# Kernel optimization log

Measured on AMD Instinct MI355X. Metric: run time of the kernel, lower is better.

The kernel has to match this reference:

```python
import jax, jax.numpy as jnp
import numpy as np

N_NODES = 50000
N_EDGES = 800000
D_IN = 64
D_OUT = 64


def setup_inputs() -> dict:
    key = jax.random.key(0)
    k1, k2, k3, k4, k5, k6 = jax.random.split(key, 6)
    feat = jax.random.normal(k1, (N_NODES, D_IN), dtype=jnp.float32)
    edge_weight = jax.random.uniform(k2, (N_EDGES, 1), dtype=jnp.float32)
    # xavier_uniform bound for [D_IN, D_OUT]
    bound = float(np.sqrt(6.0 / (D_IN + D_OUT)))
    W1 = jax.random.uniform(k3, (D_IN, D_OUT), minval=-bound, maxval=bound, dtype=jnp.float32)
    W2 = jax.random.uniform(k4, (D_IN, D_OUT), minval=-bound, maxval=bound, dtype=jnp.float32)
    src = jax.random.randint(k5, (N_EDGES,), 0, N_NODES, dtype=jnp.int64)
    dst = jax.random.randint(k6, (N_EDGES,), 0, N_NODES, dtype=jnp.int64)
    return {"feat": feat, "edge_weight": edge_weight, "W1": W1, "W2": W2, "src": src, "dst": dst}


def reference(feat, edge_weight, W1, W2, src, dst):
    # message: u_sub_e -> src feature minus (broadcast) edge weight  [E, D_IN]
    msgs = feat[src] - edge_weight
    # sum aggregation over destination nodes  [N, D_IN]
    agg = jax.ops.segment_sum(msgs, dst, num_segments=feat.shape[0])
    # dual dense projections; no activation (activation=None)
    rst = jnp.matmul(feat, W1) + jnp.matmul(agg, W2)
    return rst
```

## Files before the change

### kernel.cpp

```cpp
#include <hip/hip_runtime.h>

#define NN 50000
#define NE 800000
#define D  64
#define NB 782
#define EBLK 2048
#define NEB 391
#define CAPB 1280

typedef unsigned int u32;
typedef unsigned short u16;
typedef unsigned long long u64;
typedef __attribute__((ext_vector_type(8))) short bf16x8;
typedef __attribute__((ext_vector_type(4))) float f32x4;
typedef __attribute__((ext_vector_type(2))) float f32x2;

__device__ __forceinline__ int wave_incl_scan(int v, int lane) {
    #pragma unroll
    for (int off = 1; off < 64; off <<= 1) {
        int t = __shfl_up(v, off);
        if (lane >= off) v += t;
    }
    return v;
}

__device__ __forceinline__ u32 f2bf(float x) {
    u32 u = __float_as_uint(x);
    return (u + 0x7fffu + ((u >> 16) & 1u)) >> 16;
}

__device__ __forceinline__ bf16x8 as_bf8(uint4 u) {
    union { uint4 a; bf16x8 b; } x; x.a = u; return x.b;
}

__device__ __forceinline__ u32 pk_fp8x4(float a, float b, float c, float d) {
    int w = __builtin_amdgcn_cvt_pk_fp8_f32(a, b, 0, false);
    w = __builtin_amdgcn_cvt_pk_fp8_f32(c, d, w, true);
    return (u32)w;
}

__device__ __forceinline__ uint2 fp8x4_to_bf16x4(u32 uu) {
    f32x2 lo = __builtin_amdgcn_cvt_pk_f32_fp8((int)uu, false);
    f32x2 hi = __builtin_amdgcn_cvt_pk_f32_fp8((int)uu, true);
    uint2 r;
    r.x = f2bf(lo.x) | (f2bf(lo.y) << 16);
    r.y = f2bf(hi.x) | (f2bf(hi.y) << 16);
    return r;
}

__global__ __launch_bounds__(256) void kb_scatter(const int* __restrict__ src,
                                                  const int* __restrict__ dst,
                                                  const float* __restrict__ ew,
                                                  const float* __restrict__ feat,
                                                  u32* __restrict__ cursor,
                                                  u64* __restrict__ sorted,
                                                  uint2* __restrict__ featb8)
{
    __shared__ u32 h[NB], eb[NB], ctr[NB], gb[NB];
    __shared__ u64 buf[EBLK];
    int tid = threadIdx.x;
    for (int i = tid; i < NB; i += 256) h[i] = 0;
    __syncthreads();
    int base = blockIdx.x * EBLK;
    int n = min(EBLK, NE - base);

    u32 rd[8], rs[8], rw[8];
    #pragma unroll
    for (int j = 0; j < 8; ++j) {
        int k = tid + j * 256;
        if (k < n) {
            int e = base + k;
            rd[j] = (u32)dst[e];
            rs[j] = (u32)src[e];
            rw[j] = __float_as_uint(ew[e]);
            atomicAdd(&h[rd[j] >> 6], 1u);
        }
    }
    __syncthreads();
    if (tid < 64) {
        u32 carry = 0;
        for (int c = 0; c < 13; ++c) {
            int idx = c * 64 + tid;
            u32 v = (idx < NB) ? h[idx] : 0;
            int incl = wave_incl_scan((int)v, tid);
            if (idx < NB) { u32 e = (u32)incl - v + carry; eb[idx] = e; ctr[idx] = e; }
            carry += (u32)__shfl(incl, 63);
        }
    }
    __syncthreads();
    for (int i = tid; i < NB; i += 256) gb[i] = atomicAdd(&cursor[i], h[i]);
    __syncthreads();
    #pragma unroll
    for (int j = 0; j < 8; ++j) {
        int k = tid + j * 256;
        if (k < n) {
            u64 rec = ((u64)((rd[j] << 16) | rs[j]) << 32) | (u64)rw[j];
            u32 p = atomicAdd(&ctr[rd[j] >> 6], 1u);
            buf[p] = rec;
        }
    }
    __syncthreads();
    for (int k = tid; k < n; k += 256) {
        u64 rec = buf[k];
        u32 bin = (u32)(rec >> 54);
        u32 idx = gb[bin] + (u32)k - eb[bin];
        if (idx < CAPB) sorted[(size_t)bin * CAPB + idx] = rec;
    }

    int cbase = blockIdx.x * 1024;
    const float4* f4 = (const float4*)feat;
    #pragma unroll
    for (int j = 0; j < 4; ++j) {
        int i = cbase + j * 256 + tid;
        if (i < NN * D / 8) {
            float4 a = f4[2 * i], b = f4[2 * i + 1];
            uint2 p8;
            p8.x = pk_fp8x4(a.x, a.y, a.z, a.w);
            p8.y = pk_fp8x4(b.x, b.y, b.z, b.w);
            featb8[i] = p8;
        }
    }
}

__global__ __launch_bounds__(1024) void kcgg(
    const u64* __restrict__ sorted,
    const u32* __restrict__ cursor,
    const u32* __restrict__ fb8,
    const float* __restrict__ W1,
    const float* __restrict__ W2,
    float* __restrict__ out)
{
    __shared__ u32 hcnt[64], hbase[65], ctr[64];
    __shared__ u16 bufS[CAPB];
    __shared__ u32 bufWf[CAPB];
    __shared__ u16 aggT[64][72];
    __shared__ u16 wT[64][136];
    __shared__ float csp[4][64];
    __shared__ float csum[64];
    __shared__ float sWs[64];

    const int tid = threadIdx.x;
    const int bin = blockIdx.x;
    const int n = min((int)cursor[bin], CAPB);
    const size_t rbase = (size_t)bin * CAPB;

    for (int i = tid; i < 8192; i += 1024) {
        int k = i >> 6, c = i & 63;
        float v = (k < 64) ? W1[i] : W2[i - 4096];
        wT[c][k] = (u16)f2bf(v);
    }
    if (tid < 256) {
        int c = tid & 63, kq = tid >> 6;
        float s = 0.f;
        for (int k = kq * 16; k < kq * 16 + 16; ++k) s += W2[k * 64 + c];
        csp[kq][c] = s;
    }
    if (tid < 64) hcnt[tid] = 0;
    __syncthreads();
    if (tid < 64) csum[tid] = csp[0][tid] + csp[1][tid] + csp[2][tid] + csp[3][tid];
    for (int k = tid; k < n; k += 1024)
        atomicAdd(&hcnt[(int)(sorted[rbase + k] >> 48) & 63], 1u);
    __syncthreads();
    if (tid < 64) {
        u32 v = hcnt[tid];
        int incl = wave_incl_scan((int)v, tid);
        u32 ex = (u32)incl - v;
        hbase[tid] = ex; ctr[tid] = ex;
        if (tid == 63) hbase[64] = (u32)incl;
    }
    __syncthreads();
    for (int k = tid; k < n; k += 1024) {
        u64 rec = sorted[rbase + k];
        u32 p = atomicAdd(&ctr[(int)(rec >> 48) & 63], 1u);
        bufS[p]  = (u16)(rec >> 32);
        bufWf[p] = (u32)rec;
    }
    __syncthreads();

    const int w    = tid >> 6;
    const int lane = tid & 63;
    const int g    = lane >> 4;
    const int li   = lane & 15;
    const int ln   = w * 4 + g;

    int e   = (int)hbase[ln];
    int end = (int)hbase[ln + 1];

    if (li == 0) {
        float s = 0.f;
        for (int j = e; j < end; ++j) s += __uint_as_float(bufWf[j]);
        sWs[ln] = s;
    }

    float4 acc = make_float4(0.f, 0.f, 0.f, 0.f);
    for (; e + 7 < end; e += 8) {
        int s0 = bufS[e],     s1 = bufS[e + 1];
        int s2 = bufS[e + 2], s3 = bufS[e + 3];
        int s4 = bufS[e + 4], s5 = bufS[e + 5];
        int s6 = bufS[e + 6], s7 = bufS[e + 7];
        u32 u0 = fb8[(size_t)s0 * 16 + li];
        u32 u1 = fb8[(size_t)s1 * 16 + li];
        u32 u2 = fb8[(size_t)s2 * 16 + li];
        u32 u3 = fb8[(size_t)s3 * 16 + li];
        u32 u4 = fb8[(size_t)s4 * 16 + li];
        u32 u5 = fb8[(size_t)s5 * 16 + li];
        u32 u6 = fb8[(size_t)s6 * 16 + li];
        u32 u7 = fb8[(size_t)s7 * 16 + li];
        #pragma unroll
        for (int j = 0; j < 8; ++j) {
            u32 uu = j == 0 ? u0 : j == 1 ? u1 : j == 2 ? u2 : j == 3 ? u3
                   : j == 4 ? u4 : j == 5 ? u5 : j == 6 ? u6 : u7;
            f32x2 lo = __builtin_amdgcn_cvt_pk_f32_fp8((int)uu, false);
            f32x2 hi = __builtin_amdgcn_cvt_pk_f32_fp8((int)uu, true);
            acc.x += lo.x; acc.y += lo.y; acc.z += hi.x; acc.w += hi.y;
        }
    }
    for (; e < end; ++e) {
        u32 uu = fb8[(size_t)bufS[e] * 16 + li];
        f32x2 lo = __builtin_amdgcn_cvt_pk_f32_fp8((int)uu, false);
        f32x2 hi = __builtin_amdgcn_cvt_pk_f32_fp8((int)uu, true);
        acc.x += lo.x; acc.y += lo.y; acc.z += hi.x; acc.w += hi.y;
    }
    {
        uint2 o;
        o.x = f2bf(acc.x) | (f2bf(acc.y) << 16);
        o.y = f2bf(acc.z) | (f2bf(acc.w) << 16);
        *(uint2*)&aggT[ln][li * 4] = o;
    }
    __syncthreads();

    const int nt = w >> 2;
    const int ct = w & 3;
    const int lr = lane & 15;
    const int q  = lane >> 4;
    const int m0 = (bin << 6) + nt * 16;

    bf16x8 b0 = *(const bf16x8*)&wT[ct * 16 + lr][ 0 + q * 8];
    bf16x8 b1 = *(const bf16x8*)&wT[ct * 16 + lr][32 + q * 8];
    bf16x8 b2 = *(const bf16x8*)&wT[ct * 16 + lr][64 + q * 8];
    bf16x8 b3 = *(const bf16x8*)&wT[ct * 16 + lr][96 + q * 8];

    const size_t arow = (size_t)(m0 + lr) * 16;
    u32 f0 = fb8[arow + q * 2], f1 = fb8[arow + q * 2 + 1];
    u32 f2 = fb8[arow + 8 + q * 2], f3 = fb8[arow + 8 + q * 2 + 1];
    uint2 r0 = fp8x4_to_bf16x4(f0), r1 = fp8x4_to_bf16x4(f1);
    uint2 r2 = fp8x4_to_bf16x4(f2), r3 = fp8x4_to_bf16x4(f3);
    bf16x8 a0 = as_bf8(make_uint4(r0.x, r0.y, r1.x, r1.y));
    bf16x8 a1 = as_bf8(make_uint4(r2.x, r2.y, r3.x, r3.y));
    bf16x8 a2 = *(const bf16x8*)&aggT[nt * 16 + lr][q * 8];
    bf16x8 a3 = *(const bf16x8*)&aggT[nt * 16 + lr][32 + q * 8];

    f32x4 o4 = {0.f, 0.f, 0.f, 0.f};
    o4 = __builtin_amdgcn_mfma_f32_16x16x32_bf16(a0, b0, o4, 0, 0, 0);
    o4 = __builtin_amdgcn_mfma_f32_16x16x32_bf16(a1, b1, o4, 0, 0, 0);
    o4 = __builtin_amdgcn_mfma_f32_16x16x32_bf16(a2, b2, o4, 0, 0, 0);
    o4 = __builtin_amdgcn_mfma_f32_16x16x32_bf16(a3, b3, o4, 0, 0, 0);

    #pragma unroll
    for (int r = 0; r < 4; ++r) {
        int row = m0 + q * 4 + r;
        if (row < NN) {
            float s = sWs[nt * 16 + q * 4 + r];
            out[(size_t)row * D + ct * 16 + lr] = o4[r] - s * csum[ct * 16 + lr];
        }
    }
}

extern "C" void kernel_launch(void* const* d_in, const int* in_sizes, int n_in,
                              void* d_out, int out_size, void* d_ws, size_t ws_size,
                              hipStream_t stream)
{
    const float* feat = (const float*)d_in[0];
    const float* ew   = (const float*)d_in[1];
    const float* W1   = (const float*)d_in[2];
    const float* W2   = (const float*)d_in[3];
    const int*   src  = (const int*)  d_in[4];
    const int*   dst  = (const int*)  d_in[5];
    float* out = (float*)d_out;

    char* p = (char*)d_ws;
    size_t o = 0;
    auto take = [&](size_t bytes) { char* q = p + o; o = (o + bytes + 255) & ~(size_t)255; return q; };
    u64* sorted   = (u64*)take((size_t)NB * CAPB * 8);
    u32* cursor   = (u32*)take((size_t)NB * 4);
    uint2* featb8 = (uint2*)take((size_t)NN * D + 4096);

    hipMemsetAsync(cursor, 0, (size_t)NB * 4, stream);
    kb_scatter<<<NEB, 256, 0, stream>>>(src, dst, ew, feat, cursor, sorted,
                                        (uint2*)featb8);
    kcgg      <<<NB, 1024, 0, stream>>>(sorted, cursor, (const u32*)featb8,
                                        W1, W2, out);
}
```

Measured before the change: 55.54 us.

## Compress sorted edge records to split u32/bf16 arrays and halve gather block size

Edge records written by the scatter kernel shrink from 8 bytes to 6: the destination-local index and source go into a u32 array, and the edge weight is stored as bf16 in a separate u16 array. This cuts global write and read traffic for the intermediate buckets. The gather/GEMM kernel now runs with 512 threads per block, so each wave group handles two destination rows and two MFMA tiles, which may improve occupancy and amortise the weight staging. Storing weights as bf16 adds rounding error to the weight-sum correction term.

```diff
diff --git a/kernel.cpp b/kernel.cpp
--- a/kernel.cpp
+++ b/kernel.cpp
@@ -53,7 +53,8 @@
                                                   const float* __restrict__ ew,
                                                   const float* __restrict__ feat,
                                                   u32* __restrict__ cursor,
-                                                  u64* __restrict__ sorted,
+                                                  u32* __restrict__ sortedR,
+                                                  u16* __restrict__ sortedW,
                                                   uint2* __restrict__ featb8)
 {
     __shared__ u32 h[NB], eb[NB], ctr[NB], gb[NB];
@@ -72,7 +73,7 @@
             int e = base + k;
             rd[j] = (u32)dst[e];
             rs[j] = (u32)src[e];
-            rw[j] = __float_as_uint(ew[e]);
+            rw[j] = f2bf(ew[e]);
             atomicAdd(&h[rd[j] >> 6], 1u);
         }
     }
@@ -94,7 +95,7 @@
     for (int j = 0; j < 8; ++j) {
         int k = tid + j * 256;
         if (k < n) {
-            u64 rec = ((u64)((rd[j] << 16) | rs[j]) << 32) | (u64)rw[j];
+            u64 rec = ((u64)rd[j] << 32) | ((u64)rs[j] << 16) | (u64)rw[j];
             u32 p = atomicAdd(&ctr[rd[j] >> 6], 1u);
             buf[p] = rec;
         }
@@ -102,9 +103,14 @@
     __syncthreads();
     for (int k = tid; k < n; k += 256) {
         u64 rec = buf[k];
-        u32 bin = (u32)(rec >> 54);
+        u32 bin = (u32)(rec >> 38);
         u32 idx = gb[bin] + (u32)k - eb[bin];
-        if (idx < CAPB) sorted[(size_t)bin * CAPB + idx] = rec;
+        if (idx < CAPB) {
+            u32 dstl = (u32)(rec >> 32) & 63u;
+            u32 s    = (u32)(rec >> 16) & 0xffffu;
+            sortedR[(size_t)bin * CAPB + idx] = (dstl << 16) | s;
+            sortedW[(size_t)bin * CAPB + idx] = (u16)(rec & 0xffffu);
+        }
     }
 
     int cbase = blockIdx.x * 1024;
@@ -122,8 +128,9 @@
     }
 }
 
-__global__ __launch_bounds__(1024) void kcgg(
-    const u64* __restrict__ sorted,
+__global__ __launch_bounds__(512) void kcgg(
+    const u32* __restrict__ sortedR,
+    const u16* __restrict__ sortedW,
     const u32* __restrict__ cursor,
     const u32* __restrict__ fb8,
     const float* __restrict__ W1,
@@ -132,7 +139,7 @@
 {
     __shared__ u32 hcnt[64], hbase[65], ctr[64];
     __shared__ u16 bufS[CAPB];
-    __shared__ u32 bufWf[CAPB];
+    __shared__ u16 bufW[CAPB];
     __shared__ u16 aggT[64][72];
     __shared__ u16 wT[64][136];
     __shared__ float csp[4][64];
@@ -144,7 +151,7 @@
     const int n = min((int)cursor[bin], CAPB);
     const size_t rbase = (size_t)bin * CAPB;
 
-    for (int i = tid; i < 8192; i += 1024) {
+    for (int i = tid; i < 8192; i += 512) {
         int k = i >> 6, c = i & 63;
         float v = (k < 64) ? W1[i] : W2[i - 4096];
         wT[c][k] = (u16)f2bf(v);
@@ -158,8 +165,8 @@
     if (tid < 64) hcnt[tid] = 0;
     __syncthreads();
     if (tid < 64) csum[tid] = csp[0][tid] + csp[1][tid] + csp[2][tid] + csp[3][tid];
-    for (int k = tid; k < n; k += 1024)
-        atomicAdd(&hcnt[(int)(sorted[rbase + k] >> 48) & 63], 1u);
+    for (int k = tid; k < n; k += 512)
+        atomicAdd(&hcnt[(sortedR[rbase + k] >> 16) & 63u], 1u);
     __syncthreads();
     if (tid < 64) {
         u32 v = hcnt[tid];
@@ -169,11 +176,12 @@
         if (tid == 63) hbase[64] = (u32)incl;
     }
     __syncthreads();
-    for (int k = tid; k < n; k += 1024) {
-        u64 rec = sorted[rbase + k];
-        u32 p = atomicAdd(&ctr[(int)(rec >> 48) & 63], 1u);
-        bufS[p]  = (u16)(rec >> 32);
-        bufWf[p] = (u32)rec;
+    for (int k = tid; k < n; k += 512) {
+        u32 r = sortedR[rbase + k];
+        u16 wv = sortedW[rbase + k];
+        u32 p = atomicAdd(&ctr[(r >> 16) & 63u], 1u);
+        bufS[p] = (u16)(r & 0xffffu);
+        bufW[p] = wv;
     }
     __syncthreads();
 
@@ -181,47 +189,50 @@
     const int lane = tid & 63;
     const int g    = lane >> 4;
     const int li   = lane & 15;
-    const int ln   = w * 4 + g;
-
-    int e   = (int)hbase[ln];
-    int end = (int)hbase[ln + 1];
-
-    if (li == 0) {
-        float s = 0.f;
-        for (int j = e; j < end; ++j) s += __uint_as_float(bufWf[j]);
-        sWs[ln] = s;
-    }
-
-    float4 acc = make_float4(0.f, 0.f, 0.f, 0.f);
-    for (; e + 7 < end; e += 8) {
-        int s0 = bufS[e],     s1 = bufS[e + 1];
-        int s2 = bufS[e + 2], s3 = bufS[e + 3];
-        int s4 = bufS[e + 4], s5 = bufS[e + 5];
-        int s6 = bufS[e + 6], s7 = bufS[e + 7];
-        u32 u0 = fb8[(size_t)s0 * 16 + li];
-        u32 u1 = fb8[(size_t)s1 * 16 + li];
-        u32 u2 = fb8[(size_t)s2 * 16 + li];
-        u32 u3 = fb8[(size_t)s3 * 16 + li];
-        u32 u4 = fb8[(size_t)s4 * 16 + li];
-        u32 u5 = fb8[(size_t)s5 * 16 + li];
-        u32 u6 = fb8[(size_t)s6 * 16 + li];
-        u32 u7 = fb8[(size_t)s7 * 16 + li];
-        #pragma unroll
-        for (int j = 0; j < 8; ++j) {
-            u32 uu = j == 0 ? u0 : j == 1 ? u1 : j == 2 ? u2 : j == 3 ? u3
-                   : j == 4 ? u4 : j == 5 ? u5 : j == 6 ? u6 : u7;
+    const int gid  = w * 4 + g;
+
+    #pragma unroll
+    for (int t = 0; t < 2; ++t) {
+        const int ln = gid + 32 * t;
+        int e   = (int)hbase[ln];
+        int end = (int)hbase[ln + 1];
+
+        if (li == 0) {
+            float s = 0.f;
+            for (int j = e; j < end; ++j)
+                s += __uint_as_float((u32)bufW[j] << 16);
+            sWs[ln] = s;
+        }
+
+        float4 acc = make_float4(0.f, 0.f, 0.f, 0.f);
+        for (; e + 7 < end; e += 8) {
+            int s0 = bufS[e],     s1 = bufS[e + 1];
+            int s2 = bufS[e + 2], s3 = bufS[e + 3];
+            int s4 = bufS[e + 4], s5 = bufS[e + 5];
+            int s6 = bufS[e + 6], s7 = bufS[e + 7];
+            u32 u0 = fb8[(size_t)s0 * 16 + li];
+            u32 u1 = fb8[(size_t)s1 * 16 + li];
+            u32 u2 = fb8[(size_t)s2 * 16 + li];
+            u32 u3 = fb8[(size_t)s3 * 16 + li];
+            u32 u4 = fb8[(size_t)s4 * 16 + li];
+            u32 u5 = fb8[(size_t)s5 * 16 + li];
+            u32 u6 = fb8[(size_t)s6 * 16 + li];
+            u32 u7 = fb8[(size_t)s7 * 16 + li];
+            #pragma unroll
+            for (int j = 0; j < 8; ++j) {
+                u32 uu = j == 0 ? u0 : j == 1 ? u1 : j == 2 ? u2 : j == 3 ? u3
+                       : j == 4 ? u4 : j == 5 ? u5 : j == 6 ? u6 : u7;
+                f32x2 lo = __builtin_amdgcn_cvt_pk_f32_fp8((int)uu, false);
+                f32x2 hi = __builtin_amdgcn_cvt_pk_f32_fp8((int)uu, true);
+                acc.x += lo.x; acc.y += lo.y; acc.z += hi.x; acc.w += hi.y;
+            }
+        }
+        for (; e < end; ++e) {
+            u32 uu = fb8[(size_t)bufS[e] * 16 + li];
             f32x2 lo = __builtin_amdgcn_cvt_pk_f32_fp8((int)uu, false);
             f32x2 hi = __builtin_amdgcn_cvt_pk_f32_fp8((int)uu, true);
             acc.x += lo.x; acc.y += lo.y; acc.z += hi.x; acc.w += hi.y;
         }
-    }
-    for (; e < end; ++e) {
-        u32 uu = fb8[(size_t)bufS[e] * 16 + li];
-        f32x2 lo = __builtin_amdgcn_cvt_pk_f32_fp8((int)uu, false);
-        f32x2 hi = __builtin_amdgcn_cvt_pk_f32_fp8((int)uu, true);
-        acc.x += lo.x; acc.y += lo.y; acc.z += hi.x; acc.w += hi.y;
-    }
-    {
         uint2 o;
         o.x = f2bf(acc.x) | (f2bf(acc.y) << 16);
         o.y = f2bf(acc.z) | (f2bf(acc.w) << 16);
@@ -229,39 +240,43 @@
     }
     __syncthreads();
 
-    const int nt = w >> 2;
     const int ct = w & 3;
     const int lr = lane & 15;
     const int q  = lane >> 4;
-    const int m0 = (bin << 6) + nt * 16;
 
     bf16x8 b0 = *(const bf16x8*)&wT[ct * 16 + lr][ 0 + q * 8];
     bf16x8 b1 = *(const bf16x8*)&wT[ct * 16 + lr][32 + q * 8];
     bf16x8 b2 = *(const bf16x8*)&wT[ct * 16 + lr][64 + q * 8];
     bf16x8 b3 = *(const bf16x8*)&wT[ct * 16 + lr][96 + q * 8];
 
-    const size_t arow = (size_t)(m0 + lr) * 16;
-    u32 f0 = fb8[arow + q * 2], f1 = fb8[arow + q * 2 + 1];
-    u32 f2 = fb8[arow + 8 + q * 2], f3 = fb8[arow + 8 + q * 2 + 1];
-    uint2 r0 = fp8x4_to_bf16x4(f0), r1 = fp8x4_to_bf16x4(f1);
-    uint2 r2 = fp8x4_to_bf16x4(f2), r3 = fp8x4_to_bf16x4(f3);
-    bf16x8 a0 = as_bf8(make_uint4(r0.x, r0.y, r1.x, r1.y));
-    bf16x8 a1 = as_bf8(make_uint4(r2.x, r2.y, r3.x, r3.y));
-    bf16x8 a2 = *(const bf16x8*)&aggT[nt * 16 + lr][q * 8];
-    bf16x8 a3 = *(const bf16x8*)&aggT[nt * 16 + lr][32 + q * 8];
-
-    f32x4 o4 = {0.f, 0.f, 0.f, 0.f};
-    o4 = __builtin_amdgcn_mfma_f32_16x16x32_bf16(a0, b0, o4, 0, 0, 0);
-    o4 = __builtin_amdgcn_mfma_f32_16x16x32_bf16(a1, b1, o4, 0, 0, 0);
-    o4 = __builtin_amdgcn_mfma_f32_16x16x32_bf16(a2, b2, o4, 0, 0, 0);
-    o4 = __builtin_amdgcn_mfma_f32_16x16x32_bf16(a3, b3, o4, 0, 0, 0);
-
-    #pragma unroll
-    for (int r = 0; r < 4; ++r) {
-        int row = m0 + q * 4 + r;
-        if (row < NN) {
-            float s = sWs[nt * 16 + q * 4 + r];
-            out[(size_t)row * D + ct * 16 + lr] = o4[r] - s * csum[ct * 16 + lr];
+    #pragma unroll
+    for (int t = 0; t < 2; ++t) {
+        const int nt = (w >> 2) + 2 * t;
+        const int m0 = (bin << 6) + nt * 16;
+
+        const size_t arow = (size_t)(m0 + lr) * 16;
+        u32 f0 = fb8[arow + q * 2], f1 = fb8[arow + q * 2 + 1];
+        u32 f2 = fb8[arow + 8 + q * 2], f3 = fb8[arow + 8 + q * 2 + 1];
+        uint2 r0 = fp8x4_to_bf16x4(f0), r1 = fp8x4_to_bf16x4(f1);
+        uint2 r2 = fp8x4_to_bf16x4(f2), r3 = fp8x4_to_bf16x4(f3);
+        bf16x8 a0 = as_bf8(make_uint4(r0.x, r0.y, r1.x, r1.y));
+        bf16x8 a1 = as_bf8(make_uint4(r2.x, r2.y, r3.x, r3.y));
+        bf16x8 a2 = *(const bf16x8*)&aggT[nt * 16 + lr][q * 8];
+        bf16x8 a3 = *(const bf16x8*)&aggT[nt * 16 + lr][32 + q * 8];
+
+        f32x4 o4 = {0.f, 0.f, 0.f, 0.f};
+        o4 = __builtin_amdgcn_mfma_f32_16x16x32_bf16(a0, b0, o4, 0, 0, 0);
+        o4 = __builtin_amdgcn_mfma_f32_16x16x32_bf16(a1, b1, o4, 0, 0, 0);
+        o4 = __builtin_amdgcn_mfma_f32_16x16x32_bf16(a2, b2, o4, 0, 0, 0);
+        o4 = __builtin_amdgcn_mfma_f32_16x16x32_bf16(a3, b3, o4, 0, 0, 0);
+
+        #pragma unroll
+        for (int r = 0; r < 4; ++r) {
+            int row = m0 + q * 4 + r;
+            if (row < NN) {
+                float s = sWs[nt * 16 + q * 4 + r];
+                out[(size_t)row * D + ct * 16 + lr] = o4[r] - s * csum[ct * 16 + lr];
+            }
         }
     }
 }
@@ -281,13 +296,14 @@
     char* p = (char*)d_ws;
     size_t o = 0;
     auto take = [&](size_t bytes) { char* q = p + o; o = (o + bytes + 255) & ~(size_t)255; return q; };
-    u64* sorted   = (u64*)take((size_t)NB * CAPB * 8);
+    u32* sortedR  = (u32*)take((size_t)NB * CAPB * 4);
+    u16* sortedW  = (u16*)take((size_t)NB * CAPB * 2);
     u32* cursor   = (u32*)take((size_t)NB * 4);
     uint2* featb8 = (uint2*)take((size_t)NN * D + 4096);
 
     hipMemsetAsync(cursor, 0, (size_t)NB * 4, stream);
-    kb_scatter<<<NEB, 256, 0, stream>>>(src, dst, ew, feat, cursor, sorted,
-                                        (uint2*)featb8);
-    kcgg      <<<NB, 1024, 0, stream>>>(sorted, cursor, (const u32*)featb8,
-                                        W1, W2, out);
-}
+    kb_scatter<<<NEB, 256, 0, stream>>>(src, dst, ew, feat, cursor,
+                                        sortedR, sortedW, (uint2*)featb8);
+    kcgg      <<<NB, 512, 0, stream>>>(sortedR, sortedW, cursor,
+                                       (const u32*)featb8, W1, W2, out);
+}
```

Result: slower. 57.58 us (+3.7%).
